# Performance work log

Measured on AMD Instinct MI355X. Metric: run time of the kernel, lower is better.

Reference implementation:

```python
import jax, jax.numpy as jnp
import numpy as np
import math

N_H = 16

def _rope(x):
    # x: [b, h, n, d_k]; standard RoPE with half-split rotation
    n, d_k = x.shape[2], x.shape[3]
    inv_freq = 1.0 / (10000.0 ** (jnp.arange(0, d_k, 2, dtype=jnp.float32) / d_k))  # [d_k/2]
    freqs = jnp.arange(n, dtype=jnp.float32)[:, None] * inv_freq[None, :]            # [n, d_k/2]
    cos = jnp.concatenate([jnp.cos(freqs), jnp.cos(freqs)], axis=-1)[None, None]     # [1,1,n,d_k]
    sin = jnp.concatenate([jnp.sin(freqs), jnp.sin(freqs)], axis=-1)[None, None]
    x1, x2 = jnp.split(x, 2, axis=-1)
    rot = jnp.concatenate([-x2, x1], axis=-1)
    return x * cos + rot * sin


def setup_inputs() -> dict:
    key = jax.random.key(0)
    k1, k2, k3, k4 = jax.random.split(key, 4)
    b, n, d_m = 2, 1024, 2048
    x = jax.random.normal(k1, (b, n, d_m), dtype=jnp.float32)
    # causal mask (1 = keep, 0 = masked)
    m = jnp.tril(jnp.ones((n, n), dtype=jnp.int32))[None, None]  # [1,1,n,n]
    s = 1.0 / math.sqrt(d_m)
    Wqkv = jax.random.normal(k2, (d_m, 3 * d_m), dtype=jnp.float32) * s
    Wout = jax.random.normal(k3, (d_m, d_m), dtype=jnp.float32) * s
    bout = jax.random.normal(k4, (d_m,), dtype=jnp.float32) * 0.01
    return {"x": x, "m": m, "Wqkv": Wqkv, "Wout": Wout, "bout": bout}


def reference(x, m, Wqkv, Wout, bout):
    b, n, d = x.shape
    d_k = d // N_H
    qkv = (x @ Wqkv).reshape(b, n, 3, N_H, d_k)
    qkv = jnp.transpose(qkv, (2, 0, 3, 1, 4))  # [3, b, h, n, d_k]
    q, k, v = qkv[0], qkv[1], qkv[2]
    q, k = _rope(q), _rope(k)
    s = jnp.einsum('bhqd,bhkd->bhqk', q, k) / math.sqrt(d_k)
    s = jnp.where(m == 0, -jnp.inf, s)
    a = jax.nn.softmax(s, axis=-1)  # dropout is identity in eval / drop=0
    r = jnp.einsum('bhqk,bhkd->bhqd', a, v)
    r = jnp.transpose(r, (0, 2, 1, 3)).reshape(b, n, d)
    return r @ Wout + bout
```

## Files before the change

kernel.cpp:

```cpp
#include <hip/hip_runtime.h>
#include <math.h>

typedef unsigned short u16;
typedef unsigned int u32;
typedef __attribute__((ext_vector_type(8))) short short8;
typedef __attribute__((ext_vector_type(4))) float f32x4;

#define DEVI __device__ __forceinline__

DEVI u16 f2bf(float x) {
    union { float f; u32 u; } un; un.f = x;
    u32 u = un.u;
    return (u16)((u + 0x7fffu + ((u >> 16) & 1u)) >> 16);
}
DEVI float bf2f(u16 v) {
    union { u32 u; float f; } un; un.u = ((u32)v) << 16;
    return un.f;
}
DEVI f32x4 mfma_bf16(short8 a, short8 b, f32x4 c) {
    return __builtin_amdgcn_mfma_f32_16x16x32_bf16(a, b, c, 0, 0, 0);
}
DEVI void gload_lds16(const void* g, void* l) {
    __builtin_amdgcn_global_load_lds((const __attribute__((address_space(1))) u32*)g,
                                     (__attribute__((address_space(3))) u32*)l,
                                     16, 0, 0);
}

DEVI void transpose_tile_64(const float* __restrict__ in, u16* __restrict__ out,
                            int R, int C, int bx, int by, int tidx, u16 (*tile)[68]) {
    const int tx = tidx & 15, ty = tidx >> 4;
    const long r0 = (long)by * 64, c0 = (long)bx * 64;
#pragma unroll
    for (int p = 0; p < 4; ++p) {
        int r = ty + p * 16;
        float4 v = *(const float4*)(in + (r0 + r) * C + c0 + tx * 4);
        ushort4 o;
        o.x = f2bf(v.x); o.y = f2bf(v.y); o.z = f2bf(v.z); o.w = f2bf(v.w);
        *(ushort4*)&tile[r][tx * 4] = o;
    }
    __syncthreads();
#pragma unroll
    for (int p = 0; p < 4; ++p) {
        int rr = ty + p * 16;
        ushort4 o;
        o.x = tile[tx * 4 + 0][rr];
        o.y = tile[tx * 4 + 1][rr];
        o.z = tile[tx * 4 + 2][rr];
        o.w = tile[tx * 4 + 3][rr];
        *(ushort4*)(out + (c0 + rr) * R + r0 + tx * 4) = o;
    }
}

__global__ void k_prep(const float* __restrict__ x, const float* __restrict__ Wqkv,
                       const float* __restrict__ Wout, u16* __restrict__ x_bf,
                       u16* __restrict__ WqkvT, u16* __restrict__ WoutT) {
    __shared__ u16 tile[64][68];
    const int bid = blockIdx.x;
    if (bid < 4096) {
        long idx = ((long)bid * 256 + threadIdx.x) * 4;
        float4 v = *(const float4*)(x + idx);
        ushort4 o;
        o.x = f2bf(v.x); o.y = f2bf(v.y); o.z = f2bf(v.z); o.w = f2bf(v.w);
        *(ushort4*)(x_bf + idx) = o;
        return;
    }
    if (bid < 7168) {
        int lb = bid - 4096;
        transpose_tile_64(Wqkv, WqkvT, 2048, 6144, lb % 96, lb / 96, threadIdx.x, tile);
    } else {
        int lb = bid - 7168;
        transpose_tile_64(Wout, WoutT, 2048, 2048, lb & 31, lb >> 5, threadIdx.x, tile);
    }
}

__global__ __launch_bounds__(256, 3) void k_gemm_qkv(const u16* __restrict__ A,
                                                     const u16* __restrict__ BT,
                                                     u16* __restrict__ qb, u16* __restrict__ kb,
                                                     u16* __restrict__ vtb) {
    constexpr int K = 2048;
    __shared__ __align__(16) union SM {
        struct { u16 As[128 * 64]; u16 Bs[128 * 64]; } s;
        u16 T[128 * 132];
    } sm;
    const int tid = threadIdx.x;
    const int lane = tid & 63, wave = tid >> 6;
    const int lm = lane & 15, quad = lane >> 4;
    const int wm = wave >> 1, wn = wave & 1;
    const int bm = blockIdx.x, bn = blockIdx.y;

    f32x4 acc[4][4] = {};

    const int srow = lane >> 3;
    const int scb = (lane & 7) ^ srow;
    const long arow0 = (long)bm * 128;
    const long brow0 = (long)bn * 128;

    for (int k0 = 0; k0 < K; k0 += 64) {
        __syncthreads();
#pragma unroll
        for (int it = 0; it < 4; ++it) {
            int ch = wave * 4 + it;
            long r = ch * 8 + srow;
            gload_lds16(A + (arow0 + r) * K + k0 + scb * 8, (char*)sm.s.As + ch * 1024);
            gload_lds16(BT + (brow0 + r) * K + k0 + scb * 8, (char*)sm.s.Bs + ch * 1024);
        }
        __syncthreads();
#pragma unroll
        for (int ko = 0; ko < 2; ++ko) {
            short8 af[4], bf[4];
#pragma unroll
            for (int i = 0; i < 4; ++i) {
                int row = wm * 64 + i * 16 + lm;
                int pc = (ko * 4 + quad) ^ (lm & 7);
                af[i] = *(const short8*)&sm.s.As[row * 64 + pc * 8];
            }
#pragma unroll
            for (int j = 0; j < 4; ++j) {
                int row = wn * 64 + j * 16 + lm;
                int pc = (ko * 4 + quad) ^ (lm & 7);
                bf[j] = *(const short8*)&sm.s.Bs[row * 64 + pc * 8];
            }
#pragma unroll
            for (int i = 0; i < 4; ++i)
#pragma unroll
                for (int j = 0; j < 4; ++j)
                    acc[i][j] = mfma_bf16(af[i], bf[j], acc[i][j]);
        }
    }

    __syncthreads();
#pragma unroll
    for (int i = 0; i < 4; ++i)
#pragma unroll
        for (int j = 0; j < 4; ++j) {
            const int col = wn * 64 + j * 16 + lm;
#pragma unroll
            for (int r = 0; r < 4; ++r) {
                const int row = wm * 64 + i * 16 + quad * 4 + r;
                sm.T[row * 132 + col] = f2bf(acc[i][j][r]);
            }
        }
    __syncthreads();
    const int which = bn >> 4, h = bn & 15, b = bm >> 3;
    const int p0 = (bm & 7) * 128;
    if (which < 2) {
        u16* dst = which ? kb : qb;
        const long hb = ((long)(b * 16 + h)) * 1024;
        const int i0 = (tid * 4) & 63;
        const int pb = tid >> 4;
        float inv[4];
#pragma unroll
        for (int e = 0; e < 4; ++e)
            inv[e] = exp2f(-(float)(i0 + e) * 0.20762050593045952f);
#pragma unroll
        for (int c = 0; c < 8; ++c) {
            const int pos_l = c * 16 + pb;
            ushort4 cur = *(const ushort4*)&sm.T[pos_l * 132 + i0];
            ushort4 par = *(const ushort4*)&sm.T[pos_l * 132 + i0 + 64];
            const float pg = (float)(p0 + pos_l);
            ushort4 o1, o2;
            const u16* cp = (const u16*)&cur;
            const u16* pp = (const u16*)&par;
            u16* o1p = (u16*)&o1;
            u16* o2p = (u16*)&o2;
#pragma unroll
            for (int e = 0; e < 4; ++e) {
                float th = pg * inv[e];
                float sv = __sinf(th), cv = __cosf(th);
                float x1 = bf2f(cp[e]), x2 = bf2f(pp[e]);
                o1p[e] = f2bf(x1 * cv - x2 * sv);
                o2p[e] = f2bf(x2 * cv + x1 * sv);
            }
            const long rowb = (hb + p0 + pos_l) * 128;
            *(ushort4*)(dst + rowb + i0) = o1;
            *(ushort4*)(dst + rowb + i0 + 64) = o2;
        }
    } else {
        const long vrow = ((long)(b * 16 + h)) * 128;
#pragma unroll
        for (int c = 0; c < 8; ++c) {
            const int lin = c * 2048 + tid * 8;
            const int dk = lin >> 7;
            const int ps = lin & 127;
            ushort4 o1, o2;
            u16* o1p = (u16*)&o1;
            u16* o2p = (u16*)&o2;
#pragma unroll
            for (int e = 0; e < 4; ++e) {
                o1p[e] = sm.T[(ps + e) * 132 + dk];
                o2p[e] = sm.T[(ps + 4 + e) * 132 + dk];
            }
            u16* dst = vtb + (vrow + dk) * 1024 + p0 + ps;
            *(ushort4*)dst = o1;
            *(ushort4*)(dst + 4) = o2;
        }
    }
}

__global__ __launch_bounds__(256, 3) void k_gemm_out(const u16* __restrict__ A,
                                                     const u16* __restrict__ BT,
                                                     float* __restrict__ out,
                                                     const float* __restrict__ bias) {
    constexpr int K = 2048;
    __shared__ __align__(16) struct { u16 As[64 * 64]; u16 Bs[128 * 64]; } sm;
    const int tid = threadIdx.x;
    const int lane = tid & 63, wave = tid >> 6;
    const int lm = lane & 15, quad = lane >> 4;
    const int wm = wave >> 1, wn = wave & 1;
    const int bm = blockIdx.x, bn = blockIdx.y;

    f32x4 acc[2][4] = {};

    const int srow = lane >> 3;
    const int scb = (lane & 7) ^ srow;
    const long arow0 = (long)bm * 64;
    const long brow0 = (long)bn * 128;

    for (int k0 = 0; k0 < K; k0 += 64) {
        __syncthreads();
#pragma unroll
        for (int it = 0; it < 2; ++it) {
            int ch = wave * 2 + it;
            long r = ch * 8 + srow;
            gload_lds16(A + (arow0 + r) * K + k0 + scb * 8, (char*)sm.As + ch * 1024);
        }
#pragma unroll
        for (int it = 0; it < 4; ++it) {
            int ch = wave * 4 + it;
            long r = ch * 8 + srow;
            gload_lds16(BT + (brow0 + r) * K + k0 + scb * 8, (char*)sm.Bs + ch * 1024);
        }
        __syncthreads();
#pragma unroll
        for (int ko = 0; ko < 2; ++ko) {
            short8 af[2], bf[4];
#pragma unroll
            for (int i = 0; i < 2; ++i) {
                int row = wm * 32 + i * 16 + lm;
                int pc = (ko * 4 + quad) ^ (lm & 7);
                af[i] = *(const short8*)&sm.As[row * 64 + pc * 8];
            }
#pragma unroll
            for (int j = 0; j < 4; ++j) {
                int row = wn * 64 + j * 16 + lm;
                int pc = (ko * 4 + quad) ^ (lm & 7);
                bf[j] = *(const short8*)&sm.Bs[row * 64 + pc * 8];
            }
#pragma unroll
            for (int i = 0; i < 2; ++i)
#pragma unroll
                for (int j = 0; j < 4; ++j)
                    acc[i][j] = mfma_bf16(af[i], bf[j], acc[i][j]);
        }
    }

    float bv[4];
#pragma unroll
    for (int j = 0; j < 4; ++j) bv[j] = bias[bn * 128 + wn * 64 + j * 16 + lm];
#pragma unroll
    for (int i = 0; i < 2; ++i) {
#pragma unroll
        for (int r = 0; r < 4; ++r) {
            const int row = bm * 64 + wm * 32 + i * 16 + quad * 4 + r;
#pragma unroll
            for (int j = 0; j < 4; ++j) {
                const int col = bn * 128 + wn * 64 + j * 16 + lm;
                out[(long)row * 2048 + col] = acc[i][j][r] + bv[j];
            }
        }
    }
}

__global__ __launch_bounds__(256, 3) void k_flash(const u16* __restrict__ Q,
                                                  const u16* __restrict__ Kb,
                                                  const u16* __restrict__ VT,
                                                  u16* __restrict__ R) {
    __shared__ u16 Ks[64 * 128];
    __shared__ u16 Vs[128 * 64];
    __shared__ u16 Ps[64 * 72];
    const int tid = threadIdx.x;
    const int lane = tid & 63, wave = tid >> 6;
    const int lm = lane & 15, quad = lane >> 4;
    const int id = blockIdx.x;
    const int g = id >> 8, rem = id & 255;
    const int bh = rem >> 3, s = rem & 7;
    const int qt = g ? (15 - s) : s;
    const long qkbase = (long)bh * 1024 * 128;
    const long vtbase = (long)bh * 128 * 1024;
    const int q0 = qt * 64;

    short8 qf[4];
    {
        const u16* qrow = Q + qkbase + (long)(q0 + wave * 16 + lm) * 128 + quad * 8;
#pragma unroll
        for (int kc = 0; kc < 4; ++kc) qf[kc] = *(const short8*)(qrow + kc * 32);
    }

    f32x4 o_acc[8] = {};
    float m_i = -INFINITY, l_i = 0.f;
    const float cl2e = 0.08838834764831845f * 1.4426950408889634f;

    const int kr = lane >> 4;
    const int vr = lane >> 3;
    const int vcb = (lane & 7) ^ vr;

    for (int kt = 0; kt <= qt; ++kt) {
        __syncthreads();
        {
#pragma unroll
            for (int it = 0; it < 4; ++it) {
                int ch = wave * 4 + it;
                int krow = ch * 4 + kr;
                int kchunk = (lane & 15) ^ (krow & 15);
                gload_lds16(Kb + qkbase + (long)(kt * 64 + krow) * 128 + kchunk * 8,
                            (char*)Ks + ch * 1024);
                int vrow = ch * 8 + vr;
                gload_lds16(VT + vtbase + (long)vrow * 1024 + kt * 64 + vcb * 8,
                            (char*)Vs + ch * 1024);
            }
        }
        __syncthreads();

        f32x4 s_acc[4] = {};
#pragma unroll
        for (int kc = 0; kc < 4; ++kc) {
#pragma unroll
            for (int mi = 0; mi < 4; ++mi) {
                int row = mi * 16 + lm;
                int pc = (kc * 4 + quad) ^ lm;
                short8 ak = *(const short8*)&Ks[row * 128 + pc * 8];
                s_acc[mi] = mfma_bf16(ak, qf[kc], s_acc[mi]);
            }
        }
        float t[4][4];
        float cmax = -INFINITY;
        if (kt == qt) {
            const int qg = q0 + wave * 16 + lm;
#pragma unroll
            for (int mi = 0; mi < 4; ++mi)
#pragma unroll
                for (int r = 0; r < 4; ++r) {
                    int kg = kt * 64 + mi * 16 + quad * 4 + r;
                    float val = (kg <= qg) ? s_acc[mi][r] * cl2e : -INFINITY;
                    t[mi][r] = val;
                    cmax = fmaxf(cmax, val);
                }
        } else {
#pragma unroll
            for (int mi = 0; mi < 4; ++mi)
#pragma unroll
                for (int r = 0; r < 4; ++r) {
                    float val = s_acc[mi][r] * cl2e;
                    t[mi][r] = val;
                    cmax = fmaxf(cmax, val);
                }
        }
        cmax = fmaxf(cmax, __shfl_xor(cmax, 16));
        cmax = fmaxf(cmax, __shfl_xor(cmax, 32));
        float m_new = fmaxf(m_i, cmax);
        float alpha = exp2f(m_i - m_new);
        float csum = 0.f;
#pragma unroll
        for (int mi = 0; mi < 4; ++mi)
#pragma unroll
            for (int r = 0; r < 4; ++r) {
                float p = exp2f(t[mi][r] - m_new);
                t[mi][r] = p;
                csum += p;
            }
        csum += __shfl_xor(csum, 16);
        csum += __shfl_xor(csum, 32);
        l_i = l_i * alpha + csum;
        m_i = m_new;
#pragma unroll
        for (int mi = 0; mi < 4; ++mi) {
            ushort4 pk;
            pk.x = f2bf(t[mi][0]); pk.y = f2bf(t[mi][1]);
            pk.z = f2bf(t[mi][2]); pk.w = f2bf(t[mi][3]);
            *(ushort4*)&Ps[(wave * 16 + lm) * 72 + mi * 16 + quad * 4] = pk;
        }
        float aq[4];
#pragma unroll
        for (int r = 0; r < 4; ++r) aq[r] = __shfl(alpha, quad * 4 + r, 64);
#pragma unroll
        for (int nt = 0; nt < 8; ++nt)
#pragma unroll
            for (int r = 0; r < 4; ++r) o_acc[nt][r] *= aq[r];
#pragma unroll
        for (int kc = 0; kc < 2; ++kc) {
            short8 ap = *(const short8*)&Ps[(wave * 16 + lm) * 72 + kc * 32 + quad * 8];
#pragma unroll
            for (int nt = 0; nt < 8; ++nt) {
                int row = nt * 16 + lm;
                int pc = (kc * 4 + quad) ^ (lm & 7);
                short8 bv = *(const short8*)&Vs[row * 64 + pc * 8];
                o_acc[nt] = mfma_bf16(ap, bv, o_acc[nt]);
            }
        }
    }
    float lq[4];
#pragma unroll
    for (int r = 0; r < 4; ++r) lq[r] = __shfl(l_i, quad * 4 + r, 64);
    const int b = bh >> 4, h = bh & 15;
#pragma unroll
    for (int nt = 0; nt < 8; ++nt)
#pragma unroll
        for (int r = 0; r < 4; ++r) {
            const int pos = q0 + wave * 16 + quad * 4 + r;
            const int col = h * 128 + nt * 16 + lm;
            R[((long)b * 1024 + pos) * 2048 + col] = f2bf(o_acc[nt][r] / lq[r]);
        }
}

extern "C" void kernel_launch(void* const* d_in, const int* in_sizes, int n_in,
                              void* d_out, int out_size, void* d_ws, size_t ws_size,
                              hipStream_t stream) {
    const float* x    = (const float*)d_in[0];
    const float* Wqkv = (const float*)d_in[2];
    const float* Wout = (const float*)d_in[3];
    const float* bout = (const float*)d_in[4];
    float* out = (float*)d_out;

    char* ws = (char*)d_ws;
    u16* x_bf  = (u16*)(ws);
    u16* rbuf  = x_bf;
    u16* WqkvT = (u16*)(ws + (8L << 20));
    u16* WoutT = (u16*)(ws + (32L << 20));
    u16* qbuf  = (u16*)(ws + (40L << 20));
    u16* kbuf  = (u16*)(ws + (48L << 20));
    u16* vtbuf = (u16*)(ws + (56L << 20));

    k_prep<<<8192, 256, 0, stream>>>(x, Wqkv, Wout, x_bf, WqkvT, WoutT);
    k_gemm_qkv<<<dim3(16, 48), 256, 0, stream>>>(x_bf, WqkvT, qbuf, kbuf, vtbuf);
    k_flash<<<512, 256, 0, stream>>>(qbuf, kbuf, vtbuf, rbuf);
    k_gemm_out<<<dim3(32, 16), 256, 0, stream>>>(rbuf, WoutT, out, bout);
}
```

Before: 247.5 us.

## Double-buffer LDS tiles in output GEMM and flash attention kernels

```diff
diff --git a/kernel.cpp b/kernel.cpp
--- a/kernel.cpp
+++ b/kernel.cpp
@@ -197,12 +197,12 @@
     }
 }
 
-__global__ __launch_bounds__(256, 3) void k_gemm_out(const u16* __restrict__ A,
+__global__ __launch_bounds__(256, 2) void k_gemm_out(const u16* __restrict__ A,
                                                      const u16* __restrict__ BT,
                                                      float* __restrict__ out,
                                                      const float* __restrict__ bias) {
     constexpr int K = 2048;
-    __shared__ __align__(16) struct { u16 As[64 * 64]; u16 Bs[128 * 64]; } sm;
+    __shared__ __align__(16) struct { u16 As[2][64 * 64]; u16 Bs[2][128 * 64]; } sm;
     const int tid = threadIdx.x;
     const int lane = tid & 63, wave = tid >> 6;
     const int lm = lane & 15, quad = lane >> 4;
@@ -216,21 +216,26 @@
     const long arow0 = (long)bm * 64;
     const long brow0 = (long)bn * 128;
 
-    for (int k0 = 0; k0 < K; k0 += 64) {
-        __syncthreads();
+    auto stage = [&](int k0, int buf) {
 #pragma unroll
         for (int it = 0; it < 2; ++it) {
             int ch = wave * 2 + it;
             long r = ch * 8 + srow;
-            gload_lds16(A + (arow0 + r) * K + k0 + scb * 8, (char*)sm.As + ch * 1024);
+            gload_lds16(A + (arow0 + r) * K + k0 + scb * 8, (char*)sm.As[buf] + ch * 1024);
         }
 #pragma unroll
         for (int it = 0; it < 4; ++it) {
             int ch = wave * 4 + it;
             long r = ch * 8 + srow;
-            gload_lds16(BT + (brow0 + r) * K + k0 + scb * 8, (char*)sm.Bs + ch * 1024);
-        }
+            gload_lds16(BT + (brow0 + r) * K + k0 + scb * 8, (char*)sm.Bs[buf] + ch * 1024);
+        }
+    };
+
+    stage(0, 0);
+    for (int k0 = 0; k0 < K; k0 += 64) {
+        const int cur = (k0 >> 6) & 1;
         __syncthreads();
+        if (k0 + 64 < K) stage(k0 + 64, cur ^ 1);
 #pragma unroll
         for (int ko = 0; ko < 2; ++ko) {
             short8 af[2], bf[4];
@@ -238,13 +243,13 @@
             for (int i = 0; i < 2; ++i) {
                 int row = wm * 32 + i * 16 + lm;
                 int pc = (ko * 4 + quad) ^ (lm & 7);
-                af[i] = *(const short8*)&sm.As[row * 64 + pc * 8];
+                af[i] = *(const short8*)&sm.As[cur][row * 64 + pc * 8];
             }
 #pragma unroll
             for (int j = 0; j < 4; ++j) {
                 int row = wn * 64 + j * 16 + lm;
                 int pc = (ko * 4 + quad) ^ (lm & 7);
-                bf[j] = *(const short8*)&sm.Bs[row * 64 + pc * 8];
+                bf[j] = *(const short8*)&sm.Bs[cur][row * 64 + pc * 8];
             }
 #pragma unroll
             for (int i = 0; i < 2; ++i)
@@ -271,12 +276,12 @@
     }
 }
 
-__global__ __launch_bounds__(256, 3) void k_flash(const u16* __restrict__ Q,
+__global__ __launch_bounds__(256, 2) void k_flash(const u16* __restrict__ Q,
                                                   const u16* __restrict__ Kb,
                                                   const u16* __restrict__ VT,
                                                   u16* __restrict__ R) {
-    __shared__ u16 Ks[64 * 128];
-    __shared__ u16 Vs[128 * 64];
+    __shared__ u16 Ks[2][64 * 128];
+    __shared__ u16 Vs[2][128 * 64];
     __shared__ u16 Ps[64 * 72];
     const int tid = threadIdx.x;
     const int lane = tid & 63, wave = tid >> 6;
@@ -304,22 +309,25 @@
     const int vr = lane >> 3;
     const int vcb = (lane & 7) ^ vr;
 
+    auto stage = [&](int kt, int buf) {
+#pragma unroll
+        for (int it = 0; it < 4; ++it) {
+            int ch = wave * 4 + it;
+            int krow = ch * 4 + kr;
+            int kchunk = (lane & 15) ^ (krow & 15);
+            gload_lds16(Kb + qkbase + (long)(kt * 64 + krow) * 128 + kchunk * 8,
+                        (char*)Ks[buf] + ch * 1024);
+            int vrow = ch * 8 + vr;
+            gload_lds16(VT + vtbase + (long)vrow * 1024 + kt * 64 + vcb * 8,
+                        (char*)Vs[buf] + ch * 1024);
+        }
+    };
+
+    stage(0, 0);
     for (int kt = 0; kt <= qt; ++kt) {
+        const int cur = kt & 1;
         __syncthreads();
-        {
-#pragma unroll
-            for (int it = 0; it < 4; ++it) {
-                int ch = wave * 4 + it;
-                int krow = ch * 4 + kr;
-                int kchunk = (lane & 15) ^ (krow & 15);
-                gload_lds16(Kb + qkbase + (long)(kt * 64 + krow) * 128 + kchunk * 8,
-                            (char*)Ks + ch * 1024);
-                int vrow = ch * 8 + vr;
-                gload_lds16(VT + vtbase + (long)vrow * 1024 + kt * 64 + vcb * 8,
-                            (char*)Vs + ch * 1024);
-            }
-        }
-        __syncthreads();
+        if (kt < qt) stage(kt + 1, cur ^ 1);
 
         f32x4 s_acc[4] = {};
 #pragma unroll
@@ -328,7 +336,7 @@
             for (int mi = 0; mi < 4; ++mi) {
                 int row = mi * 16 + lm;
                 int pc = (kc * 4 + quad) ^ lm;
-                short8 ak = *(const short8*)&Ks[row * 128 + pc * 8];
+                short8 ak = *(const short8*)&Ks[cur][row * 128 + pc * 8];
                 s_acc[mi] = mfma_bf16(ak, qf[kc], s_acc[mi]);
             }
         }
@@ -393,7 +401,7 @@
             for (int nt = 0; nt < 8; ++nt) {
                 int row = nt * 16 + lm;
                 int pc = (kc * 4 + quad) ^ (lm & 7);
-                short8 bv = *(const short8*)&Vs[row * 64 + pc * 8];
+                short8 bv = *(const short8*)&Vs[cur][row * 64 + pc * 8];
                 o_acc[nt] = mfma_bf16(ap, bv, o_acc[nt]);
             }
         }
```

After: 242.8 us. Within noise of the previous version (-1.9%).
